# Kernel tuning notes

Measured on AMD Instinct MI355X. Metric: run time of the kernel, lower is better.

## Reference

```python
import jax, jax.numpy as jnp
import numpy as np
from jax import lax

B, T, C, H, W = 256, 1024, 8, 64, 128  # batch, knots, input_channels, hidden_dim, mlp width


def _natural_cubic_coeffs(y):
    """y: np.ndarray [..., T] sampled at uniform knots t=0..T-1 (h=1).
    Returns per-interval coeffs a,b,c,d each [..., T-1] for
    X(t_i + s) = a + b s + c s^2 + d s^3, natural boundary conditions."""
    n = y.shape[-1] - 2  # inner second derivatives
    rhs = 6.0 * (y[..., 2:] - 2.0 * y[..., 1:-1] + y[..., :-2])
    # Thomas algorithm for tridiag(1, 4, 1), vectorized over leading dims
    cp = np.zeros(n, dtype=np.float64)
    dp = np.zeros(y.shape[:-1] + (n,), dtype=np.float64)
    cp[0] = 1.0 / 4.0
    dp[..., 0] = rhs[..., 0] / 4.0
    for i in range(1, n):
        m = 4.0 - cp[i - 1]
        cp[i] = 1.0 / m
        dp[..., i] = (rhs[..., i] - dp[..., i - 1]) / m
    M_in = np.zeros_like(dp)
    M_in[..., n - 1] = dp[..., n - 1]
    for i in range(n - 2, -1, -1):
        M_in[..., i] = dp[..., i] - cp[i] * M_in[..., i + 1]
    M = np.zeros_like(y, dtype=np.float64)
    M[..., 1:-1] = M_in
    a = y[..., :-1]
    b = (y[..., 1:] - y[..., :-1]) - (2.0 * M[..., :-1] + M[..., 1:]) / 6.0
    c = M[..., :-1] / 2.0
    d = (M[..., 1:] - M[..., :-1]) / 6.0
    return a, b, c, d


def setup_inputs() -> dict:
    key = jax.random.key(0)
    ks = jax.random.split(key, 8)
    # underlying path samples [B, C, T]
    y = np.asarray(jax.random.normal(ks[0], (B, C, T), dtype=jnp.float32), dtype=np.float64)
    y = np.cumsum(y, axis=-1) * 0.1  # smooth-ish random walk path
    a, b, c, d = _natural_cubic_coeffs(y)
    to_btc = lambda z: jnp.asarray(np.moveaxis(z, 1, 2), dtype=jnp.float32)  # [B, T-1, C]
    s = 0.05
    return {
        "coeff_a": to_btc(a),
        "coeff_b": to_btc(b),
        "coeff_c": to_btc(c),
        "coeff_d": to_btc(d),
        "W_init": jax.random.normal(ks[1], (C, H), dtype=jnp.float32) * s,
        "b_init": jnp.zeros((H,), dtype=jnp.float32),
        "W1": jax.random.normal(ks[2], (H, W), dtype=jnp.float32) * s,
        "b1": jnp.zeros((W,), dtype=jnp.float32),
        "W2": jax.random.normal(ks[3], (W, H * C), dtype=jnp.float32) * s,
        "b2": jnp.zeros((H * C,), dtype=jnp.float32),
    }


def reference(coeff_a, coeff_b, coeff_c, coeff_d, W_init, b_init, W1, b1, W2, b2):
    # z0 = initial_network(X(t0)); X(t0) = a[:, 0]
    x0 = coeff_a[:, 0, :]                      # [B, C]
    z0 = x0 @ W_init + b_init                  # [B, H]
    # dX over each unit interval, derivative evaluated at interval midpoint s=0.5:
    # X'(s) = b + 2 c s + 3 d s^2 -> b + c + 0.75 d ; times h=1
    dX = coeff_b + coeff_c + 0.75 * coeff_d    # [B, T-1, C]

    def step(z, dx):
        h = jax.nn.relu(z @ W1 + b1)           # [B, W]
        f = jnp.tanh(h @ W2 + b2).reshape(z.shape[0], H, C)  # vector field [B, H, C]
        z = z + jnp.einsum('bhc,bc->bh', f, dx)
        return z, z

    _, zs = lax.scan(step, z0, jnp.moveaxis(dX, 1, 0))  # zs: [T-1, B, H]
    z_traj = jnp.concatenate([z0[:, None, :], jnp.moveaxis(zs, 0, 1)], axis=1)  # [B, T, H]
    return z_traj
```

## Files before the change

### kernel.cpp

```cpp
#include <hip/hip_runtime.h>


#define NB    256
#define TT    1024
#define NSTEP 1023
#define CC    8
#define HH    64
#define WW    128
#define KK    512

typedef float v2f __attribute__((ext_vector_type(2)));

__device__ __forceinline__ float fast_tanh(float x) {
    float e = __expf(2.0f * x);
    return 1.0f - 2.0f * __builtin_amdgcn_rcpf(e + 1.0f);
}

__global__ __launch_bounds__(512, 2)
void cde_kernel(const float* __restrict__ ca, const float* __restrict__ cb,
                const float* __restrict__ cc, const float* __restrict__ cd,
                const float* __restrict__ Wi, const float* __restrict__ bi,
                const float* __restrict__ W1, const float* __restrict__ b1,
                const float* __restrict__ W2, const float* __restrict__ b2,
                float* __restrict__ out)
{
    const int b = blockIdx.x;
    const int t = threadIdx.x;

    __shared__ __align__(16) float z_lds[HH];
    __shared__ __align__(16) float h_lds[WW];
    __shared__ __align__(16) float dx_all[NSTEP * CC];

    v2f w2c[64];
#pragma unroll
    for (int m = 0; m < 64; ++m) {
        v2f w = { W2[(2 * m) * KK + t], W2[(2 * m + 1) * KK + t] };
        w2c[m] = w;
    }
#pragma unroll
    for (int m = 0; m < 64; ++m) asm volatile("" : "+v"(w2c[m]));
    const float b2r = b2[t];

    const int jA = t >> 2;
    const int gA = t & 3;
    v2f w1r[8];
#pragma unroll
    for (int q = 0; q < 8; ++q) {
        int i0 = gA * 16 + 2 * q;
        v2f w = { W1[i0 * WW + jA], W1[(i0 + 1) * WW + jA] };
        w1r[q] = w;
    }
#pragma unroll
    for (int q = 0; q < 8; ++q) asm volatile("" : "+v"(w1r[q]));
    const float b1r = b1[jA];

    {
        const size_t base = (size_t)b * NSTEP * CC;
        for (int i = t; i < NSTEP * CC; i += 512)
            dx_all[i] = cb[base + i] + cc[base + i] + 0.75f * cd[base + i];
    }

    if (t < HH) {
        float acc = bi[t];
#pragma unroll
        for (int c = 0; c < CC; ++c)
            acc = fmaf(ca[(size_t)b * NSTEP * CC + c], Wi[c * HH + t], acc);
        z_lds[t] = acc;
        out[((size_t)b * TT) * HH + t] = acc;
    }
    __syncthreads();

    const float4* z4 = reinterpret_cast<const float4*>(z_lds);
    const float4* h4 = reinterpret_cast<const float4*>(h_lds);

#pragma unroll 1
    for (int s = 0; s < NSTEP; ++s) {
        v2f pa = { 0.f, 0.f }, pb = { 0.f, 0.f };
#pragma unroll
        for (int q4 = 0; q4 < 4; ++q4) {
            float4 zq = z4[gA * 4 + q4];
            v2f zlo = { zq.x, zq.y };
            v2f zhi = { zq.z, zq.w };
            pa = __builtin_elementwise_fma(zlo, w1r[2 * q4 + 0], pa);
            pb = __builtin_elementwise_fma(zhi, w1r[2 * q4 + 1], pb);
        }
        v2f ps = pa + pb;
        float p = ps.x + ps.y;
        p += __shfl_xor(p, 1);
        p += __shfl_xor(p, 2);
        if (gA == 0) h_lds[jA] = fmaxf(p + b1r, 0.0f);
        __syncthreads();

        v2f o0 = {0,0}, o1 = {0,0}, o2 = {0,0}, o3 = {0,0};
#pragma unroll
        for (int q = 0; q < 8; ++q) {
            float4 ha = h4[4 * q + 0];
            float4 hb = h4[4 * q + 1];
            float4 hc = h4[4 * q + 2];
            float4 hd = h4[4 * q + 3];
            v2f a0 = { ha.x, ha.y }, a1 = { ha.z, ha.w };
            v2f b0 = { hb.x, hb.y }, b1v = { hb.z, hb.w };
            v2f c0 = { hc.x, hc.y }, c1 = { hc.z, hc.w };
            v2f d0 = { hd.x, hd.y }, d1 = { hd.z, hd.w };
            o0 = __builtin_elementwise_fma(a0,  w2c[8 * q + 0], o0);
            o1 = __builtin_elementwise_fma(a1,  w2c[8 * q + 1], o1);
            o2 = __builtin_elementwise_fma(b0,  w2c[8 * q + 2], o2);
            o3 = __builtin_elementwise_fma(b1v, w2c[8 * q + 3], o3);
            o0 = __builtin_elementwise_fma(c0,  w2c[8 * q + 4], o0);
            o1 = __builtin_elementwise_fma(c1,  w2c[8 * q + 5], o1);
            o2 = __builtin_elementwise_fma(d0,  w2c[8 * q + 6], o2);
            o3 = __builtin_elementwise_fma(d1,  w2c[8 * q + 7], o3);
        }
        v2f oo = (o0 + o1) + (o2 + o3);
        float ok = oo.x + oo.y;
        float f  = fast_tanh(ok + b2r);

        float val = f * dx_all[s * CC + (t & 7)];
        val += __shfl_xor(val, 1);
        val += __shfl_xor(val, 2);
        val += __shfl_xor(val, 4);
        if ((t & 7) == 0) {
            int h = t >> 3;
            float zn = z_lds[h] + val;
            z_lds[h] = zn;
            out[((size_t)b * TT + (s + 1)) * HH + h] = zn;
        }
        __syncthreads();
    }
}

extern "C" void kernel_launch(void* const* d_in, const int* in_sizes, int n_in,
                              void* d_out, int out_size, void* d_ws, size_t ws_size,
                              hipStream_t stream) {
    const float* ca = (const float*)d_in[0];
    const float* cb = (const float*)d_in[1];
    const float* cc = (const float*)d_in[2];
    const float* cd = (const float*)d_in[3];
    const float* Wi = (const float*)d_in[4];
    const float* bi = (const float*)d_in[5];
    const float* W1 = (const float*)d_in[6];
    const float* b1 = (const float*)d_in[7];
    const float* W2 = (const float*)d_in[8];
    const float* b2 = (const float*)d_in[9];
    float* out = (float*)d_out;

    hipLaunchKernelGGL(cde_kernel, dim3(NB), dim3(512), 0, stream,
                       ca, cb, cc, cd, Wi, bi, W1, b1, W2, b2, out);
}
```

Baseline: 993.1 us.

## Split W2 matvec across 4-lane groups with padded LDS and DPP reductions

Restructures the second matvec so each thread in a quad handles a quarter of the hidden vector for four outputs. Partial sums are then combined with DPP quad-permute adds, and the h buffer is padded into four rows so the lanes read distinct LDS regions. Intra-quad shuffles elsewhere are also replaced with DPP moves. The aim is to cut LDS broadcast-read traffic per step: each thread now reads 32 floats instead of 128. The cost is extra reduction adds and selects per step.

```diff
diff --git a/kernel.cpp b/kernel.cpp
--- a/kernel.cpp
+++ b/kernel.cpp
@@ -16,6 +16,17 @@
     return 1.0f - 2.0f * __builtin_amdgcn_rcpf(e + 1.0f);
 }
 
+__device__ __forceinline__ float qadd1(float x) {
+    int yi = __builtin_amdgcn_mov_dpp(__builtin_bit_cast(int, x),
+                                      0xB1, 0xF, 0xF, true);
+    return x + __builtin_bit_cast(float, yi);
+}
+__device__ __forceinline__ float qadd2(float x) {
+    int yi = __builtin_amdgcn_mov_dpp(__builtin_bit_cast(int, x),
+                                      0x4E, 0xF, 0xF, true);
+    return x + __builtin_bit_cast(float, yi);
+}
+
 __global__ __launch_bounds__(512, 2)
 void cde_kernel(const float* __restrict__ ca, const float* __restrict__ cb,
                 const float* __restrict__ cc, const float* __restrict__ cd,
@@ -28,17 +39,31 @@
     const int t = threadIdx.x;
 
     __shared__ __align__(16) float z_lds[HH];
-    __shared__ __align__(16) float h_lds[WW];
+    __shared__ __align__(16) float h_pad[4][36];
     __shared__ __align__(16) float dx_all[NSTEP * CC];
 
-    v2f w2c[64];
+    const int gB = t & 3;
+    const int kb = t & ~3;
+
+    v2f w2a[8][4], w2b[8][4];
 #pragma unroll
-    for (int m = 0; m < 64; ++m) {
-        v2f w = { W2[(2 * m) * KK + t], W2[(2 * m + 1) * KK + t] };
-        w2c[m] = w;
+    for (int ch = 0; ch < 8; ++ch) {
+        int i0 = 32 * gB + 4 * ch;
+#pragma unroll
+        for (int kk = 0; kk < 4; ++kk) {
+            v2f a = { W2[(i0 + 0) * KK + kb + kk], W2[(i0 + 1) * KK + kb + kk] };
+            v2f c = { W2[(i0 + 2) * KK + kb + kk], W2[(i0 + 3) * KK + kb + kk] };
+            w2a[ch][kk] = a;
+            w2b[ch][kk] = c;
+        }
     }
 #pragma unroll
-    for (int m = 0; m < 64; ++m) asm volatile("" : "+v"(w2c[m]));
+    for (int ch = 0; ch < 8; ++ch)
+#pragma unroll
+        for (int kk = 0; kk < 4; ++kk) {
+            asm volatile("" : "+v"(w2a[ch][kk]));
+            asm volatile("" : "+v"(w2b[ch][kk]));
+        }
     const float b2r = b2[t];
 
     const int jA = t >> 2;
@@ -71,7 +96,6 @@
     __syncthreads();
 
     const float4* z4 = reinterpret_cast<const float4*>(z_lds);
-    const float4* h4 = reinterpret_cast<const float4*>(h_lds);
 
 #pragma unroll 1
     for (int s = 0; s < NSTEP; ++s) {
@@ -86,38 +110,42 @@
         }
         v2f ps = pa + pb;
         float p = ps.x + ps.y;
-        p += __shfl_xor(p, 1);
-        p += __shfl_xor(p, 2);
-        if (gA == 0) h_lds[jA] = fmaxf(p + b1r, 0.0f);
+        p = qadd1(p);
+        p = qadd2(p);
+        if (gA == 0) h_pad[jA >> 5][jA & 31] = fmaxf(p + b1r, 0.0f);
         __syncthreads();
 
-        v2f o0 = {0,0}, o1 = {0,0}, o2 = {0,0}, o3 = {0,0};
+        const float4* hp = reinterpret_cast<const float4*>(&h_pad[gB][0]);
+        v2f a0 = {0,0}, a1 = {0,0}, a2 = {0,0}, a3 = {0,0};
 #pragma unroll
-        for (int q = 0; q < 8; ++q) {
-            float4 ha = h4[4 * q + 0];
-            float4 hb = h4[4 * q + 1];
-            float4 hc = h4[4 * q + 2];
-            float4 hd = h4[4 * q + 3];
-            v2f a0 = { ha.x, ha.y }, a1 = { ha.z, ha.w };
-            v2f b0 = { hb.x, hb.y }, b1v = { hb.z, hb.w };
-            v2f c0 = { hc.x, hc.y }, c1 = { hc.z, hc.w };
-            v2f d0 = { hd.x, hd.y }, d1 = { hd.z, hd.w };
-            o0 = __builtin_elementwise_fma(a0,  w2c[8 * q + 0], o0);
-            o1 = __builtin_elementwise_fma(a1,  w2c[8 * q + 1], o1);
-            o2 = __builtin_elementwise_fma(b0,  w2c[8 * q + 2], o2);
-            o3 = __builtin_elementwise_fma(b1v, w2c[8 * q + 3], o3);
-            o0 = __builtin_elementwise_fma(c0,  w2c[8 * q + 4], o0);
-            o1 = __builtin_elementwise_fma(c1,  w2c[8 * q + 5], o1);
-            o2 = __builtin_elementwise_fma(d0,  w2c[8 * q + 6], o2);
-            o3 = __builtin_elementwise_fma(d1,  w2c[8 * q + 7], o3);
+        for (int ch = 0; ch < 8; ++ch) {
+            float4 hv = hp[ch];
+            v2f h01 = { hv.x, hv.y };
+            v2f h23 = { hv.z, hv.w };
+            a0 = __builtin_elementwise_fma(h01, w2a[ch][0], a0);
+            a1 = __builtin_elementwise_fma(h01, w2a[ch][1], a1);
+            a2 = __builtin_elementwise_fma(h01, w2a[ch][2], a2);
+            a3 = __builtin_elementwise_fma(h01, w2a[ch][3], a3);
+            a0 = __builtin_elementwise_fma(h23, w2b[ch][0], a0);
+            a1 = __builtin_elementwise_fma(h23, w2b[ch][1], a1);
+            a2 = __builtin_elementwise_fma(h23, w2b[ch][2], a2);
+            a3 = __builtin_elementwise_fma(h23, w2b[ch][3], a3);
         }
-        v2f oo = (o0 + o1) + (o2 + o3);
-        float ok = oo.x + oo.y;
+        float o0 = a0.x + a0.y;
+        float o1 = a1.x + a1.y;
+        float o2 = a2.x + a2.y;
+        float o3 = a3.x + a3.y;
+        o0 = qadd2(qadd1(o0));
+        o1 = qadd2(qadd1(o1));
+        o2 = qadd2(qadd1(o2));
+        o3 = qadd2(qadd1(o3));
+        float ok = (gB & 2) ? ((gB & 1) ? o3 : o2)
+                            : ((gB & 1) ? o1 : o0);
         float f  = fast_tanh(ok + b2r);
 
         float val = f * dx_all[s * CC + (t & 7)];
-        val += __shfl_xor(val, 1);
-        val += __shfl_xor(val, 2);
+        val = qadd1(val);
+        val = qadd2(val);
         val += __shfl_xor(val, 4);
         if ((t & 7) == 0) {
             int h = t >> 3;
```

After: 826.7 us. 16.8% less time.

## Split per-step MLP across 1024 threads with DPP/swizzle transpose-reduce

Applied to the files above, without the earlier changes.

Doubles the block to 1024 threads and repartitions both matvecs. Each thread now holds an 8x8 slice of W2 (over 8 hidden and 8 output columns) and a 1/8 slice of W1. Partial sums are combined through a butterfly transpose-reduction built from DPP moves and ds_swizzle instead of __shfl_xor, and the LDS buffers are padded. The aim is to shorten the per-step serial dependency chain and cut register pressure per thread. In exchange, each block runs 16 waves, occupancy drops to one block per CU, and synchronisation now spans more waves.

```diff
diff --git a/kernel.cpp b/kernel.cpp
--- a/kernel.cpp
+++ b/kernel.cpp
@@ -16,7 +16,26 @@
     return 1.0f - 2.0f * __builtin_amdgcn_rcpf(e + 1.0f);
 }
 
-__global__ __launch_bounds__(512, 2)
+__device__ __forceinline__ float dppx1(float x) {
+    return __builtin_bit_cast(float, __builtin_amdgcn_mov_dpp(
+        __builtin_bit_cast(int, x), 0xB1, 0xF, 0xF, true));
+}
+__device__ __forceinline__ float dppx2(float x) {
+    return __builtin_bit_cast(float, __builtin_amdgcn_mov_dpp(
+        __builtin_bit_cast(int, x), 0x4E, 0xF, 0xF, true));
+}
+__device__ __forceinline__ float swz4(float x) {
+    return __builtin_bit_cast(float, __builtin_amdgcn_ds_swizzle(
+        __builtin_bit_cast(int, x), 0x101F));
+}
+__device__ __forceinline__ float swz8(float x) {
+    return __builtin_bit_cast(float, __builtin_amdgcn_ds_swizzle(
+        __builtin_bit_cast(int, x), 0x201F));
+}
+__device__ __forceinline__ v2f dppx1v(v2f a) { v2f r; r.x = dppx1(a.x); r.y = dppx1(a.y); return r; }
+__device__ __forceinline__ v2f dppx2v(v2f a) { v2f r; r.x = dppx2(a.x); r.y = dppx2(a.y); return r; }
+
+__global__ __launch_bounds__(1024)
 void cde_kernel(const float* __restrict__ ca, const float* __restrict__ cb,
                 const float* __restrict__ cc, const float* __restrict__ cd,
                 const float* __restrict__ Wi, const float* __restrict__ bi,
@@ -27,36 +46,47 @@
     const int b = blockIdx.x;
     const int t = threadIdx.x;
 
-    __shared__ __align__(16) float z_lds[HH];
-    __shared__ __align__(16) float h_lds[WW];
+    __shared__ __align__(16) float z_pad[8][12];
+    __shared__ __align__(16) float h_pad[16][12];
     __shared__ __align__(16) float dx_all[NSTEP * CC];
 
-    v2f w2c[64];
-#pragma unroll
-    for (int m = 0; m < 64; ++m) {
-        v2f w = { W2[(2 * m) * KK + t], W2[(2 * m + 1) * KK + t] };
-        w2c[m] = w;
-    }
-#pragma unroll
-    for (int m = 0; m < 64; ++m) asm volatile("" : "+v"(w2c[m]));
-    const float b2r = b2[t];
-
-    const int jA = t >> 2;
-    const int gA = t & 3;
-    v2f w1r[8];
-#pragma unroll
-    for (int q = 0; q < 8; ++q) {
-        int i0 = gA * 16 + 2 * q;
-        v2f w = { W1[i0 * WW + jA], W1[(i0 + 1) * WW + jA] };
-        w1r[q] = w;
-    }
-#pragma unroll
-    for (int q = 0; q < 8; ++q) asm volatile("" : "+v"(w1r[q]));
+    const int g   = t >> 4;
+    const int icB = t & 15;
+    const bool bit0 = (t & 1), bit1 = (t & 2), bit2 = (t & 4);
+
+    v2f w2f[8][4];
+#pragma unroll
+    for (int ii = 0; ii < 8; ++ii) {
+        const float* wrow = W2 + (size_t)(8 * icB + ii) * KK + 8 * g;
+#pragma unroll
+        for (int p = 0; p < 4; ++p) {
+            v2f w = { wrow[p], wrow[p + 4] };
+            w2f[ii][p] = w;
+        }
+    }
+#pragma unroll
+    for (int ii = 0; ii < 8; ++ii)
+#pragma unroll
+        for (int p = 0; p < 4; ++p)
+            asm volatile("" : "+v"(w2f[ii][p]));
+    const float b2r = b2[8 * g + (icB & 7)];
+
+    const int jA  = t >> 3;
+    const int icA = t & 7;
+    v2f w1A[4];
+#pragma unroll
+    for (int q = 0; q < 4; ++q) {
+        v2f w = { W1[(8 * icA + 2 * q) * WW + jA],
+                  W1[(8 * icA + 2 * q + 1) * WW + jA] };
+        w1A[q] = w;
+    }
+#pragma unroll
+    for (int q = 0; q < 4; ++q) asm volatile("" : "+v"(w1A[q]));
     const float b1r = b1[jA];
 
     {
         const size_t base = (size_t)b * NSTEP * CC;
-        for (int i = t; i < NSTEP * CC; i += 512)
+        for (int i = t; i < NSTEP * CC; i += 1024)
             dx_all[i] = cb[base + i] + cc[base + i] + 0.75f * cd[base + i];
     }
 
@@ -65,66 +95,103 @@
 #pragma unroll
         for (int c = 0; c < CC; ++c)
             acc = fmaf(ca[(size_t)b * NSTEP * CC + c], Wi[c * HH + t], acc);
-        z_lds[t] = acc;
-        out[((size_t)b * TT) * HH + t] = acc;
+        z_pad[t >> 3][t & 7] = acc;
+        out[(size_t)b * TT * HH + t] = acc;
     }
     __syncthreads();
 
-    const float4* z4 = reinterpret_cast<const float4*>(z_lds);
-    const float4* h4 = reinterpret_cast<const float4*>(h_lds);
+    float* haddr = &h_pad[jA >> 3][jA & 7];
+    float* zaddr = &z_pad[g >> 3][g & 7];
+    float* outp  = out + (size_t)b * TT * HH + HH + g;
 
 #pragma unroll 1
     for (int s = 0; s < NSTEP; ++s) {
-        v2f pa = { 0.f, 0.f }, pb = { 0.f, 0.f };
-#pragma unroll
-        for (int q4 = 0; q4 < 4; ++q4) {
-            float4 zq = z4[gA * 4 + q4];
-            v2f zlo = { zq.x, zq.y };
-            v2f zhi = { zq.z, zq.w };
-            pa = __builtin_elementwise_fma(zlo, w1r[2 * q4 + 0], pa);
-            pb = __builtin_elementwise_fma(zhi, w1r[2 * q4 + 1], pb);
+        float4 za = *reinterpret_cast<const float4*>(&z_pad[icA][0]);
+        float4 zb = *reinterpret_cast<const float4*>(&z_pad[icA][4]);
+        v2f accA = { 0.f, 0.f };
+        { v2f zp = { za.x, za.y }; accA = __builtin_elementwise_fma(zp, w1A[0], accA); }
+        { v2f zp = { za.z, za.w }; accA = __builtin_elementwise_fma(zp, w1A[1], accA); }
+        { v2f zp = { zb.x, zb.y }; accA = __builtin_elementwise_fma(zp, w1A[2], accA); }
+        { v2f zp = { zb.z, zb.w }; accA = __builtin_elementwise_fma(zp, w1A[3], accA); }
+        float p = accA.x + accA.y;
+        p += dppx1(p);
+        p += dppx2(p);
+        p += swz4(p);
+        if (icA == 0) *haddr = fmaxf(p + b1r, 0.0f);
+        __syncthreads();
+
+        float4 ha = *reinterpret_cast<const float4*>(&h_pad[icB][0]);
+        float4 hb = *reinterpret_cast<const float4*>(&h_pad[icB][4]);
+        v2f A0 = {0,0}, A1 = {0,0}, A2 = {0,0}, A3 = {0,0};
+        {
+            v2f hs;
+            hs.x = ha.x; hs.y = ha.x;
+            A0 = __builtin_elementwise_fma(hs, w2f[0][0], A0);
+            A1 = __builtin_elementwise_fma(hs, w2f[0][1], A1);
+            A2 = __builtin_elementwise_fma(hs, w2f[0][2], A2);
+            A3 = __builtin_elementwise_fma(hs, w2f[0][3], A3);
+            hs.x = ha.y; hs.y = ha.y;
+            A0 = __builtin_elementwise_fma(hs, w2f[1][0], A0);
+            A1 = __builtin_elementwise_fma(hs, w2f[1][1], A1);
+            A2 = __builtin_elementwise_fma(hs, w2f[1][2], A2);
+            A3 = __builtin_elementwise_fma(hs, w2f[1][3], A3);
+            hs.x = ha.z; hs.y = ha.z;
+            A0 = __builtin_elementwise_fma(hs, w2f[2][0], A0);
+            A1 = __builtin_elementwise_fma(hs, w2f[2][1], A1);
+            A2 = __builtin_elementwise_fma(hs, w2f[2][2], A2);
+            A3 = __builtin_elementwise_fma(hs, w2f[2][3], A3);
+            hs.x = ha.w; hs.y = ha.w;
+            A0 = __builtin_elementwise_fma(hs, w2f[3][0], A0);
+            A1 = __builtin_elementwise_fma(hs, w2f[3][1], A1);
+            A2 = __builtin_elementwise_fma(hs, w2f[3][2], A2);
+            A3 = __builtin_elementwise_fma(hs, w2f[3][3], A3);
+            hs.x = hb.x; hs.y = hb.x;
+            A0 = __builtin_elementwise_fma(hs, w2f[4][0], A0);
+            A1 = __builtin_elementwise_fma(hs, w2f[4][1], A1);
+            A2 = __builtin_elementwise_fma(hs, w2f[4][2], A2);
+            A3 = __builtin_elementwise_fma(hs, w2f[4][3], A3);
+            hs.x = hb.y; hs.y = hb.y;
+            A0 = __builtin_elementwise_fma(hs, w2f[5][0], A0);
+            A1 = __builtin_elementwise_fma(hs, w2f[5][1], A1);
+            A2 = __builtin_elementwise_fma(hs, w2f[5][2], A2);
+            A3 = __builtin_elementwise_fma(hs, w2f[5][3], A3);
+            hs.x = hb.z; hs.y = hb.z;
+            A0 = __builtin_elementwise_fma(hs, w2f[6][0], A0);
+            A1 = __builtin_elementwise_fma(hs, w2f[6][1], A1);
+            A2 = __builtin_elementwise_fma(hs, w2f[6][2], A2);
+            A3 = __builtin_elementwise_fma(hs, w2f[6][3], A3);
+            hs.x = hb.w; hs.y = hb.w;
+            A0 = __builtin_elementwise_fma(hs, w2f[7][0], A0);
+            A1 = __builtin_elementwise_fma(hs, w2f[7][1], A1);
+            A2 = __builtin_elementwise_fma(hs, w2f[7][2], A2);
+            A3 = __builtin_elementwise_fma(hs, w2f[7][3], A3);
         }
-        v2f ps = pa + pb;
-        float p = ps.x + ps.y;
-        p += __shfl_xor(p, 1);
-        p += __shfl_xor(p, 2);
-        if (gA == 0) h_lds[jA] = fmaxf(p + b1r, 0.0f);
-        __syncthreads();
-
-        v2f o0 = {0,0}, o1 = {0,0}, o2 = {0,0}, o3 = {0,0};
-#pragma unroll
-        for (int q = 0; q < 8; ++q) {
-            float4 ha = h4[4 * q + 0];
-            float4 hb = h4[4 * q + 1];
-            float4 hc = h4[4 * q + 2];
-            float4 hd = h4[4 * q + 3];
-            v2f a0 = { ha.x, ha.y }, a1 = { ha.z, ha.w };
-            v2f b0 = { hb.x, hb.y }, b1v = { hb.z, hb.w };
-            v2f c0 = { hc.x, hc.y }, c1 = { hc.z, hc.w };
-            v2f d0 = { hd.x, hd.y }, d1 = { hd.z, hd.w };
-            o0 = __builtin_elementwise_fma(a0,  w2c[8 * q + 0], o0);
-            o1 = __builtin_elementwise_fma(a1,  w2c[8 * q + 1], o1);
-            o2 = __builtin_elementwise_fma(b0,  w2c[8 * q + 2], o2);
-            o3 = __builtin_elementwise_fma(b1v, w2c[8 * q + 3], o3);
-            o0 = __builtin_elementwise_fma(c0,  w2c[8 * q + 4], o0);
-            o1 = __builtin_elementwise_fma(c1,  w2c[8 * q + 5], o1);
-            o2 = __builtin_elementwise_fma(d0,  w2c[8 * q + 6], o2);
-            o3 = __builtin_elementwise_fma(d1,  w2c[8 * q + 7], o3);
+        v2f snda = bit0 ? A0 : A1;
+        v2f sndb = bit0 ? A2 : A3;
+        v2f kpa  = bit0 ? A1 : A0;
+        v2f kpb  = bit0 ? A3 : A2;
+        v2f B0 = kpa + dppx1v(snda);
+        v2f B1 = kpb + dppx1v(sndb);
+        v2f snd2 = bit1 ? B0 : B1;
+        v2f kp2  = bit1 ? B1 : B0;
+        v2f Cv = kp2 + dppx2v(snd2);
+        float snd3 = bit2 ? Cv.x : Cv.y;
+        float kp3  = bit2 ? Cv.y : Cv.x;
+        float o = kp3 + swz4(snd3);
+        o += swz8(o);
+
+        float f = fast_tanh(o + b2r);
+
+        float val = f * dx_all[s * CC + (t & 7)];
+        val += dppx1(val);
+        val += dppx2(val);
+        val += swz4(val);
+        if (icB == 0) {
+            float zn = *zaddr + val;
+            *zaddr = zn;
+            *outp = zn;
         }
-        v2f oo = (o0 + o1) + (o2 + o3);
-        float ok = oo.x + oo.y;
-        float f  = fast_tanh(ok + b2r);
-
-        float val = f * dx_all[s * CC + (t & 7)];
-        val += __shfl_xor(val, 1);
-        val += __shfl_xor(val, 2);
-        val += __shfl_xor(val, 4);
-        if ((t & 7) == 0) {
-            int h = t >> 3;
-            float zn = z_lds[h] + val;
-            z_lds[h] = zn;
-            out[((size_t)b * TT + (s + 1)) * HH + h] = zn;
-        }
+        outp += HH;
         __syncthreads();
     }
 }
@@ -144,6 +211,6 @@
     const float* b2 = (const float*)d_in[9];
     float* out = (float*)d_out;
 
-    hipLaunchKernelGGL(cde_kernel, dim3(NB), dim3(512), 0, stream,
+    hipLaunchKernelGGL(cde_kernel, dim3(NB), dim3(1024), 0, stream,
                        ca, cb, cc, cd, Wi, bi, W1, b1, W2, b2, out);
 }
```

Result: slower. 1.055 ms (+6.2%).

## Split W2 matvec over k-slices with register transpose-reduce and DPP shuffles

Applied to the files above, without the earlier changes.

Each thread now owns a 16-element slice of h across 8 output columns instead of all 128 h values for one column. That lets it read only 4 float4 from a padded LDS row rather than 32 broadcast reads. The partial sums are combined with a butterfly transpose-reduction using DPP row permutes and ds_swizzle, and the reductions that used shfl_xor now use DPP too. Packed FMAs are forced through inline asm, and launch bounds drop to one block per CU. The aim is to cut LDS traffic and shuffle latency in the serial per-step chain, at the cost of extra select and reduction instructions.

```diff
diff --git a/kernel.cpp b/kernel.cpp
--- a/kernel.cpp
+++ b/kernel.cpp
@@ -11,12 +11,31 @@
 
 typedef float v2f __attribute__((ext_vector_type(2)));
 
+__device__ __forceinline__ void pk_fma(v2f& acc, v2f a, v2f b) {
+    asm("v_pk_fma_f32 %0, %1, %2, %0" : "+v"(acc) : "v"(a), "v"(b));
+}
+
 __device__ __forceinline__ float fast_tanh(float x) {
     float e = __expf(2.0f * x);
     return 1.0f - 2.0f * __builtin_amdgcn_rcpf(e + 1.0f);
 }
 
-__global__ __launch_bounds__(512, 2)
+__device__ __forceinline__ float dppx1(float x) {
+    return __builtin_bit_cast(float, __builtin_amdgcn_mov_dpp(
+        __builtin_bit_cast(int, x), 0xB1, 0xF, 0xF, true));
+}
+__device__ __forceinline__ float dppx2(float x) {
+    return __builtin_bit_cast(float, __builtin_amdgcn_mov_dpp(
+        __builtin_bit_cast(int, x), 0x4E, 0xF, 0xF, true));
+}
+__device__ __forceinline__ float swz4(float x) {
+    return __builtin_bit_cast(float, __builtin_amdgcn_ds_swizzle(
+        __builtin_bit_cast(int, x), 0x101F));
+}
+__device__ __forceinline__ v2f dppx1v(v2f a) { v2f r; r.x = dppx1(a.x); r.y = dppx1(a.y); return r; }
+__device__ __forceinline__ v2f dppx2v(v2f a) { v2f r; r.x = dppx2(a.x); r.y = dppx2(a.y); return r; }
+
+__global__ __launch_bounds__(512, 1)
 void cde_kernel(const float* __restrict__ ca, const float* __restrict__ cb,
                 const float* __restrict__ cc, const float* __restrict__ cd,
                 const float* __restrict__ Wi, const float* __restrict__ bi,
@@ -28,30 +47,42 @@
     const int t = threadIdx.x;
 
     __shared__ __align__(16) float z_lds[HH];
-    __shared__ __align__(16) float h_lds[WW];
+    __shared__ __align__(16) float h_pad[8][20];
     __shared__ __align__(16) float dx_all[NSTEP * CC];
 
-    v2f w2c[64];
+    const int g8 = t >> 3;
+    const int l  = t & 7;
+    const bool bit0 = (t & 1), bit1 = (t & 2), bit2 = (t & 4);
+
+    v2f w2p[8][8];
 #pragma unroll
-    for (int m = 0; m < 64; ++m) {
-        v2f w = { W2[(2 * m) * KK + t], W2[(2 * m + 1) * KK + t] };
-        w2c[m] = w;
+    for (int ii2 = 0; ii2 < 8; ++ii2) {
+        const float* r0 = W2 + (size_t)(16 * l + 2 * ii2) * KK + 8 * g8;
+        const float* r1 = r0 + KK;
+#pragma unroll
+        for (int p = 0; p < 8; ++p) {
+            v2f w = { r0[p], r1[p] };
+            w2p[ii2][p] = w;
+        }
     }
 #pragma unroll
-    for (int m = 0; m < 64; ++m) asm volatile("" : "+v"(w2c[m]));
+    for (int ii2 = 0; ii2 < 8; ++ii2)
+#pragma unroll
+        for (int p = 0; p < 8; ++p)
+            asm volatile("" : "+v"(w2p[ii2][p]));
     const float b2r = b2[t];
 
     const int jA = t >> 2;
     const int gA = t & 3;
-    v2f w1r[8];
+    v2f w1A[8];
 #pragma unroll
     for (int q = 0; q < 8; ++q) {
-        int i0 = gA * 16 + 2 * q;
-        v2f w = { W1[i0 * WW + jA], W1[(i0 + 1) * WW + jA] };
-        w1r[q] = w;
+        v2f w = { W1[(16 * gA + 2 * q) * WW + jA],
+                  W1[(16 * gA + 2 * q + 1) * WW + jA] };
+        w1A[q] = w;
     }
 #pragma unroll
-    for (int q = 0; q < 8; ++q) asm volatile("" : "+v"(w1r[q]));
+    for (int q = 0; q < 8; ++q) asm volatile("" : "+v"(w1A[q]));
     const float b1r = b1[jA];
 
     {
@@ -66,65 +97,78 @@
         for (int c = 0; c < CC; ++c)
             acc = fmaf(ca[(size_t)b * NSTEP * CC + c], Wi[c * HH + t], acc);
         z_lds[t] = acc;
-        out[((size_t)b * TT) * HH + t] = acc;
+        out[(size_t)b * TT * HH + t] = acc;
     }
     __syncthreads();
 
     const float4* z4 = reinterpret_cast<const float4*>(z_lds);
-    const float4* h4 = reinterpret_cast<const float4*>(h_lds);
+    float* outp = out + (size_t)b * TT * HH + HH + g8;
 
 #pragma unroll 1
     for (int s = 0; s < NSTEP; ++s) {
-        v2f pa = { 0.f, 0.f }, pb = { 0.f, 0.f };
-#pragma unroll
-        for (int q4 = 0; q4 < 4; ++q4) {
-            float4 zq = z4[gA * 4 + q4];
-            v2f zlo = { zq.x, zq.y };
-            v2f zhi = { zq.z, zq.w };
-            pa = __builtin_elementwise_fma(zlo, w1r[2 * q4 + 0], pa);
-            pb = __builtin_elementwise_fma(zhi, w1r[2 * q4 + 1], pb);
-        }
-        v2f ps = pa + pb;
-        float p = ps.x + ps.y;
-        p += __shfl_xor(p, 1);
-        p += __shfl_xor(p, 2);
-        if (gA == 0) h_lds[jA] = fmaxf(p + b1r, 0.0f);
+        float4 za = z4[gA * 4 + 0];
+        float4 zb = z4[gA * 4 + 1];
+        float4 zc = z4[gA * 4 + 2];
+        float4 zd = z4[gA * 4 + 3];
+        v2f accA = { 0.f, 0.f };
+        { v2f zp = { za.x, za.y }; pk_fma(accA, zp, w1A[0]); }
+        { v2f zp = { za.z, za.w }; pk_fma(accA, zp, w1A[1]); }
+        { v2f zp = { zb.x, zb.y }; pk_fma(accA, zp, w1A[2]); }
+        { v2f zp = { zb.z, zb.w }; pk_fma(accA, zp, w1A[3]); }
+        { v2f zp = { zc.x, zc.y }; pk_fma(accA, zp, w1A[4]); }
+        { v2f zp = { zc.z, zc.w }; pk_fma(accA, zp, w1A[5]); }
+        { v2f zp = { zd.x, zd.y }; pk_fma(accA, zp, w1A[6]); }
+        { v2f zp = { zd.z, zd.w }; pk_fma(accA, zp, w1A[7]); }
+        float p = accA.x + accA.y;
+        p += dppx1(p);
+        p += dppx2(p);
+        if (gA == 0) h_pad[jA >> 4][jA & 15] = fmaxf(p + b1r, 0.0f);
         __syncthreads();
 
-        v2f o0 = {0,0}, o1 = {0,0}, o2 = {0,0}, o3 = {0,0};
+        const float4* hp = reinterpret_cast<const float4*>(&h_pad[l][0]);
+        float4 h0 = hp[0], h1 = hp[1], h2 = hp[2], h3 = hp[3];
+        v2f hpr[8];
+        hpr[0].x = h0.x; hpr[0].y = h0.y;  hpr[1].x = h0.z; hpr[1].y = h0.w;
+        hpr[2].x = h1.x; hpr[2].y = h1.y;  hpr[3].x = h1.z; hpr[3].y = h1.w;
+        hpr[4].x = h2.x; hpr[4].y = h2.y;  hpr[5].x = h2.z; hpr[5].y = h2.w;
+        hpr[6].x = h3.x; hpr[6].y = h3.y;  hpr[7].x = h3.z; hpr[7].y = h3.w;
+        v2f tmp[8];
 #pragma unroll
-        for (int q = 0; q < 8; ++q) {
-            float4 ha = h4[4 * q + 0];
-            float4 hb = h4[4 * q + 1];
-            float4 hc = h4[4 * q + 2];
-            float4 hd = h4[4 * q + 3];
-            v2f a0 = { ha.x, ha.y }, a1 = { ha.z, ha.w };
-            v2f b0 = { hb.x, hb.y }, b1v = { hb.z, hb.w };
-            v2f c0 = { hc.x, hc.y }, c1 = { hc.z, hc.w };
-            v2f d0 = { hd.x, hd.y }, d1 = { hd.z, hd.w };
-            o0 = __builtin_elementwise_fma(a0,  w2c[8 * q + 0], o0);
-            o1 = __builtin_elementwise_fma(a1,  w2c[8 * q + 1], o1);
-            o2 = __builtin_elementwise_fma(b0,  w2c[8 * q + 2], o2);
-            o3 = __builtin_elementwise_fma(b1v, w2c[8 * q + 3], o3);
-            o0 = __builtin_elementwise_fma(c0,  w2c[8 * q + 4], o0);
-            o1 = __builtin_elementwise_fma(c1,  w2c[8 * q + 5], o1);
-            o2 = __builtin_elementwise_fma(d0,  w2c[8 * q + 6], o2);
-            o3 = __builtin_elementwise_fma(d1,  w2c[8 * q + 7], o3);
+        for (int p2 = 0; p2 < 8; ++p2) { tmp[p2].x = 0.f; tmp[p2].y = 0.f; }
+#pragma unroll
+        for (int ii2 = 0; ii2 < 8; ++ii2)
+#pragma unroll
+            for (int p2 = 0; p2 < 8; ++p2)
+                pk_fma(tmp[p2], hpr[ii2], w2p[ii2][p2]);
+        v2f Ov0 = { tmp[0].x + tmp[0].y, tmp[4].x + tmp[4].y };
+        v2f Ov1 = { tmp[1].x + tmp[1].y, tmp[5].x + tmp[5].y };
+        v2f Ov2 = { tmp[2].x + tmp[2].y, tmp[6].x + tmp[6].y };
+        v2f Ov3 = { tmp[3].x + tmp[3].y, tmp[7].x + tmp[7].y };
+        v2f snda = bit0 ? Ov0 : Ov1;
+        v2f kpa  = bit0 ? Ov1 : Ov0;
+        v2f sndb = bit0 ? Ov2 : Ov3;
+        v2f kpb  = bit0 ? Ov3 : Ov2;
+        v2f B0 = kpa + dppx1v(snda);
+        v2f B1 = kpb + dppx1v(sndb);
+        v2f snd2 = bit1 ? B0 : B1;
+        v2f kp2  = bit1 ? B1 : B0;
+        v2f Cv = kp2 + dppx2v(snd2);
+        float snd3 = bit2 ? Cv.x : Cv.y;
+        float kp3  = bit2 ? Cv.y : Cv.x;
+        float o = kp3 + swz4(snd3);
+
+        float f = fast_tanh(o + b2r);
+
+        float val = f * dx_all[s * CC + l];
+        val += dppx1(val);
+        val += dppx2(val);
+        val += swz4(val);
+        if (l == 0) {
+            float zn = z_lds[g8] + val;
+            z_lds[g8] = zn;
+            *outp = zn;
         }
-        v2f oo = (o0 + o1) + (o2 + o3);
-        float ok = oo.x + oo.y;
-        float f  = fast_tanh(ok + b2r);
-
-        float val = f * dx_all[s * CC + (t & 7)];
-        val += __shfl_xor(val, 1);
-        val += __shfl_xor(val, 2);
-        val += __shfl_xor(val, 4);
-        if ((t & 7) == 0) {
-            int h = t >> 3;
-            float zn = z_lds[h] + val;
-            z_lds[h] = zn;
-            out[((size_t)b * TT + (s + 1)) * HH + h] = zn;
-        }
+        outp += HH;
         __syncthreads();
     }
 }
```

Result: faster. 953.4 us (-4.0%).
